# Kernel optimization log

Measured on AMD Instinct MI355X. Metric: run time of the kernel, lower is better.

## Reference

```python
import jax, jax.numpy as jnp
import numpy as np

# dims (match init_kwargs / input_specs)
B, T, IN, H, OUT, BR = 128, 250, 700, 512, 20, 4
VTH, DT, WARMUP = 1.0, 1.0, 10


@jax.custom_vjp
def spike_fn(v):
    # Heaviside spike with surrogate gradient (ActFun_adp style)
    return (v > 0.0).astype(v.dtype)

def _spike_fwd(v):
    return spike_fn(v), v

def _spike_bwd(v, g):
    gamma, lens = 0.5, 0.5  # gaussian surrogate
    return (g * gamma * jnp.exp(-v * v / (2.0 * lens * lens)),)

spike_fn.defvjp(_spike_fwd, _spike_bwd)


def make_mask(rng, out_dim, in_dim, branch):
    # each output neuron's branch j sees a disjoint random slice of inputs
    m = np.zeros((out_dim * branch, in_dim), np.float32)
    seg = in_dim // branch
    for i in range(out_dim):
        perm = rng.permutation(in_dim)
        for j in range(branch):
            m[i * branch + j, perm[j * seg:(j + 1) * seg]] = 1.0
    return jnp.asarray(m)


def setup_inputs() -> dict:
    key = jax.random.key(0)
    ks = jax.random.split(key, 12)
    rng = np.random.default_rng(0)
    lim1 = 1.0 / np.sqrt(IN)
    lim2 = 1.0 / np.sqrt(H)
    return {
        "x": jax.random.uniform(ks[0], (B, T, IN), dtype=jnp.float32),
        "W1": jax.random.uniform(ks[1], (H * BR, IN), minval=-lim1, maxval=lim1),
        "b1": jax.random.uniform(ks[2], (H * BR,), minval=-lim1, maxval=lim1),
        "tau_m1": jax.random.uniform(ks[3], (H,), minval=0.0, maxval=4.0),
        "tau_n1": jax.random.uniform(ks[4], (H, BR), minval=0.0, maxval=4.0),
        "mask1": make_mask(rng, H, IN, BR),
        "W2": jax.random.uniform(ks[5], (H * BR, H), minval=-lim2, maxval=lim2),
        "b2": jax.random.uniform(ks[6], (H * BR,), minval=-lim2, maxval=lim2),
        "tau_m2": jax.random.uniform(ks[7], (H,), minval=0.0, maxval=4.0),
        "tau_n2": jax.random.uniform(ks[8], (H, BR), minval=0.0, maxval=4.0),
        "mask2": make_mask(rng, H, H, BR),
        "Wo": jax.random.uniform(ks[9], (OUT, H), minval=-lim2, maxval=lim2),
        "bo": jax.random.uniform(ks[10], (OUT,), minval=-lim2, maxval=lim2),
        "tau_mo": jax.random.uniform(ks[11], (OUT,), minval=0.0, maxval=4.0),
    }


def reference(x, W1, b1, tau_m1, tau_n1, mask1, W2, b2, tau_m2, tau_n2, mask2, Wo, bo, tau_mo):
    beta1 = jax.nn.sigmoid(tau_n1)   # [H,BR] dendritic decay
    alpha1 = jax.nn.sigmoid(tau_m1)  # [H]   membrane decay
    beta2 = jax.nn.sigmoid(tau_n2)
    alpha2 = jax.nn.sigmoid(tau_m2)
    alpha_o = jax.nn.sigmoid(tau_mo)  # [OUT]
    Wm1 = W1 * mask1  # dendritic branch connectivity mask
    Wm2 = W2 * mask2
    Bsz = x.shape[0]
    Hd, Br = tau_n1.shape
    Od = tau_mo.shape[0]

    init = (jnp.zeros((Bsz, Hd, Br)), jnp.zeros((Bsz, Hd)), jnp.zeros((Bsz, Hd)),
            jnp.zeros((Bsz, Hd, Br)), jnp.zeros((Bsz, Hd)), jnp.zeros((Bsz, Hd)),
            jnp.zeros((Bsz, Od)))

    def step(c, xt):
        d1, m1, s1, d2, m2, s2, mo = c
        # layer 1: dendritic filter then LIF membrane with soft reset
        d1 = beta1 * d1 + (1.0 - beta1) * (xt @ Wm1.T + b1).reshape(Bsz, Hd, Br)
        m1 = m1 * alpha1 + (1.0 - alpha1) * DT * d1.sum(-1) - VTH * s1
        s1 = spike_fn(m1 - VTH)
        # layer 2
        d2 = beta2 * d2 + (1.0 - beta2) * (s1 @ Wm2.T + b2).reshape(Bsz, Hd, Br)
        m2 = m2 * alpha2 + (1.0 - alpha2) * DT * d2.sum(-1) - VTH * s2
        s2 = spike_fn(m2 - VTH)
        # leaky readout integrator (no spiking)
        mo = mo * alpha_o + (1.0 - alpha_o) * DT * (s2 @ Wo.T + bo)
        return (d1, m1, s1, d2, m2, s2, mo), jax.nn.softmax(mo, axis=1)

    _, ys = jax.lax.scan(step, init, jnp.swapaxes(x, 0, 1))  # ys: [T,B,OUT]
    # readout_mode == 'sum_softmax': skip steps i <= warmup_steps, sum the rest
    return ys[WARMUP + 1:].sum(0)
```

## Files before the change

### kernel.cpp

```cpp
#include <hip/hip_runtime.h>
#include <math.h>
#include <stdint.h>

#define B_    128
#define T_    250
#define IN_   700
#define INP_  704
#define H_    512
#define OUT_  20
#define BR_   4
#define HB_   2048
#define WARM_ 10
#define VTH_  1.0f
#define TC_   125
#define TP_   128
#define MP_   16384

typedef __attribute__((ext_vector_type(8)))  _Float16 half8;
typedef __attribute__((ext_vector_type(4)))  float f32x4;
typedef __attribute__((ext_vector_type(16))) float f32x16;
typedef __attribute__((ext_vector_type(4)))  int i32x4;
typedef __attribute__((ext_vector_type(16))) int i32x16;
typedef const __attribute__((address_space(1))) void* gptr_t;
typedef __attribute__((address_space(3))) void* lptr_t;

__global__ __launch_bounds__(256)
void w1prep_kernel(const float* __restrict__ W, const float* __restrict__ M,
                   _Float16* __restrict__ w0, _Float16* __restrict__ w1) {
    int i = blockIdx.x * 256 + threadIdx.x;
    if (i >= HB_ * INP_) return;
    int r = i / INP_, c = i - r * INP_;
    float v = (c < IN_) ? W[(size_t)r * IN_ + c] * M[(size_t)r * IN_ + c] : 0.f;
    _Float16 h0 = (_Float16)v;
    w0[i] = h0;
    w1[i] = (_Float16)(v - (float)h0);
}

__global__ __launch_bounds__(256)
void w2prep_kernel(const float* __restrict__ W, const float* __restrict__ M,
                   int8_t* __restrict__ p2, int8_t* __restrict__ p1,
                   int8_t* __restrict__ p0) {
    int i = blockIdx.x * 256 + threadIdx.x;
    if (i >= HB_ * H_) return;
    float v = W[i] * M[i];
    int q = (int)lrintf(v * 67108864.f);
    int b0 = (int)(int8_t)(q & 0xFF);  q = (q - b0) >> 8;
    int b1 = (int)(int8_t)(q & 0xFF);  int b2 = (q - b1) >> 8;
    p0[i] = (int8_t)b0; p1[i] = (int8_t)b1; p2[i] = (int8_t)b2;
}

__global__ __launch_bounds__(256)
void woprep_kernel(const float* __restrict__ Wo, _Float16* __restrict__ wo0,
                   _Float16* __restrict__ wo1) {
    int i = blockIdx.x * 256 + threadIdx.x;
    if (i >= 32 * H_) return;
    int n = i >> 9;
    float v = (n < OUT_) ? Wo[(size_t)n * H_ + (i & (H_ - 1))] : 0.f;
    _Float16 h0 = (_Float16)v;
    wo0[i] = h0;
    wo1[i] = (_Float16)(v - (float)h0);
}

__global__ __launch_bounds__(256)
void convx_kernel(const float* __restrict__ x, _Float16* __restrict__ x0,
                  _Float16* __restrict__ x1, int t0) {
    int i = blockIdx.x * 256 + threadIdx.x;
    if (i >= MP_ * INP_) return;
    int r = i / INP_, c = i - r * INP_;
    int bb = r >> 7, tl = r & (TP_ - 1);
    float v = (tl < TC_ && c < IN_) ? x[((size_t)bb * T_ + t0 + tl) * IN_ + c] : 0.f;
    _Float16 h0 = (_Float16)v;
    x0[i] = h0;
    x1[i] = (_Float16)(v - (float)h0);
}

__global__ void zero_kernel(float* __restrict__ p, int n4) {
    int i = blockIdx.x * blockDim.x + threadIdx.x;
    if (i < n4) ((float4*)p)[i] = make_float4(0.f, 0.f, 0.f, 0.f);
}

__global__ __launch_bounds__(256)
void l1_fused_kernel(const _Float16* __restrict__ x0, const _Float16* __restrict__ x1,
                     const _Float16* __restrict__ w0, const _Float16* __restrict__ w1,
                     const float* __restrict__ bias,
                     float* __restrict__ dst, float* __restrict__ mst,
                     float* __restrict__ spst, int8_t* __restrict__ sout,
                     const float* __restrict__ tau_m, const float* __restrict__ tau_n) {
    __shared__ alignas(16) char SMEM[69632];
    _Float16* S    = (_Float16*)SMEM;
    float*    curS = (float*)SMEM;
    int8_t*   sbuf = (int8_t*)(SMEM + 65536);

    const int tid  = threadIdx.x;
    const int wave = tid >> 6, lane = tid & 63;
    const int bb = blockIdx.y;
    const int bm = bb * TP_, bn = blockIdx.x * 128;

    const int    srow  = tid >> 2;
    const int    skoff = (((tid & 3) ^ ((srow >> 1) & 3)) * 8);
    const size_t aoff0 = (size_t)(bm + srow) * INP_ + skoff;
    const size_t aoff1 = aoff0 + (size_t)64 * INP_;
    const size_t boff0 = (size_t)(bn + srow) * INP_ + skoff;
    const size_t boff1 = boff0 + (size_t)64 * INP_;
    const int lo = wave * 512;

    const int wm = wave & 1, wn = wave >> 1;
    const int row = lane & 31;
    const int khq = lane >> 5;
    const int key = (lane >> 1) & 3;
    const int cK0 = ((0 + khq) ^ key) * 8;
    const int cK1 = ((2 + khq) ^ key) * 8;

    f32x16 acc[2][2] = {};

    auto stage = [&](int kt, int base) {
        const int k0 = kt * 32;
        _Float16* Sb = S + base;
        __builtin_amdgcn_global_load_lds((gptr_t)(x0 + aoff0 + k0), (lptr_t)(Sb + lo),          16, 0, 0);
        __builtin_amdgcn_global_load_lds((gptr_t)(x0 + aoff1 + k0), (lptr_t)(Sb + 2048  + lo),  16, 0, 0);
        __builtin_amdgcn_global_load_lds((gptr_t)(x1 + aoff0 + k0), (lptr_t)(Sb + 4096  + lo),  16, 0, 0);
        __builtin_amdgcn_global_load_lds((gptr_t)(x1 + aoff1 + k0), (lptr_t)(Sb + 6144  + lo),  16, 0, 0);
        __builtin_amdgcn_global_load_lds((gptr_t)(w0 + boff0 + k0), (lptr_t)(Sb + 8192  + lo),  16, 0, 0);
        __builtin_amdgcn_global_load_lds((gptr_t)(w0 + boff1 + k0), (lptr_t)(Sb + 10240 + lo),  16, 0, 0);
        __builtin_amdgcn_global_load_lds((gptr_t)(w1 + boff0 + k0), (lptr_t)(Sb + 12288 + lo),  16, 0, 0);
        __builtin_amdgcn_global_load_lds((gptr_t)(w1 + boff1 + k0), (lptr_t)(Sb + 14336 + lo),  16, 0, 0);
    };

    auto compute = [&](int base) {
        const _Float16* A0b = S + base;
        const _Float16* A1b = A0b + 4096;
        const _Float16* B0b = A0b + 8192;
        const _Float16* B1b = A0b + 12288;
        half8 a0f[2][2], a1f[2][2], b0f[2][2], b1f[2][2];
#pragma unroll
        for (int mt = 0; mt < 2; mt++) {
            const _Float16* ar = &A0b[(wm * 64 + mt * 32 + row) * 32];
            a0f[mt][0] = *(const half8*)&ar[cK0];
            a0f[mt][1] = *(const half8*)&ar[cK1];
        }
#pragma unroll
        for (int nt = 0; nt < 2; nt++) {
            const _Float16* br = &B0b[(wn * 64 + nt * 32 + row) * 32];
            b0f[nt][0] = *(const half8*)&br[cK0];
            b0f[nt][1] = *(const half8*)&br[cK1];
        }
        __builtin_amdgcn_s_setprio(1);
#pragma unroll
        for (int ks = 0; ks < 2; ks++)
#pragma unroll
            for (int mt = 0; mt < 2; mt++)
#pragma unroll
                for (int nt = 0; nt < 2; nt++)
                    acc[mt][nt] = __builtin_amdgcn_mfma_f32_32x32x16_f16(
                        a0f[mt][ks], b0f[nt][ks], acc[mt][nt], 0, 0, 0);
        __builtin_amdgcn_s_setprio(0);
#pragma unroll
        for (int nt = 0; nt < 2; nt++) {
            const _Float16* br = &B1b[(wn * 64 + nt * 32 + row) * 32];
            b1f[nt][0] = *(const half8*)&br[cK0];
            b1f[nt][1] = *(const half8*)&br[cK1];
        }
        __builtin_amdgcn_s_setprio(1);
#pragma unroll
        for (int ks = 0; ks < 2; ks++)
#pragma unroll
            for (int mt = 0; mt < 2; mt++)
#pragma unroll
                for (int nt = 0; nt < 2; nt++)
                    acc[mt][nt] = __builtin_amdgcn_mfma_f32_32x32x16_f16(
                        a0f[mt][ks], b1f[nt][ks], acc[mt][nt], 0, 0, 0);
        __builtin_amdgcn_s_setprio(0);
#pragma unroll
        for (int mt = 0; mt < 2; mt++) {
            const _Float16* ar = &A1b[(wm * 64 + mt * 32 + row) * 32];
            a1f[mt][0] = *(const half8*)&ar[cK0];
            a1f[mt][1] = *(const half8*)&ar[cK1];
        }
        __builtin_amdgcn_s_setprio(1);
#pragma unroll
        for (int ks = 0; ks < 2; ks++)
#pragma unroll
            for (int mt = 0; mt < 2; mt++)
#pragma unroll
                for (int nt = 0; nt < 2; nt++)
                    acc[mt][nt] = __builtin_amdgcn_mfma_f32_32x32x16_f16(
                        a1f[mt][ks], b0f[nt][ks], acc[mt][nt], 0, 0, 0);
        __builtin_amdgcn_s_setprio(0);
    };

    stage(0, 0);
    asm volatile("s_waitcnt vmcnt(0)" ::: "memory");
    __builtin_amdgcn_s_barrier();

    int cur = 0;
    for (int kt = 0; kt < INP_ / 32 - 1; kt++) {
        const int base = cur * 16384;
        stage(kt + 1, base ^ 16384);
        compute(base);
        asm volatile("s_waitcnt vmcnt(0) lgkmcnt(0)" ::: "memory");
        __builtin_amdgcn_s_barrier();
        cur ^= 1;
    }
    compute(cur * 16384);
    __syncthreads();

    const int col = lane & 31;
    const int rb  = 4 * (lane >> 5);
#pragma unroll
    for (int nt = 0; nt < 2; nt++) {
        const int lcol = wn * 64 + nt * 32 + col;
        const float bv = bias[bn + lcol];
#pragma unroll
        for (int mt = 0; mt < 2; mt++) {
#pragma unroll
            for (int reg = 0; reg < 16; reg++) {
                const int trow = wm * 64 + mt * 32 + (reg & 3) + 8 * (reg >> 2) + rb;
                curS[trow * 128 + lcol] = acc[mt][nt][reg] + bv;
            }
        }
    }
    __syncthreads();

    if (tid < 32) {
        const int hg   = blockIdx.x * 32 + tid;
        const int sidx = bb * H_ + hg;
        float alpha = 1.f / (1.f + expf(-tau_m[hg]));
        float4 tn = ((const float4*)tau_n)[hg];
        float4 beta;
        beta.x = 1.f / (1.f + expf(-tn.x));
        beta.y = 1.f / (1.f + expf(-tn.y));
        beta.z = 1.f / (1.f + expf(-tn.z));
        beta.w = 1.f / (1.f + expf(-tn.w));
        float4 d = ((const float4*)dst)[sidx];
        float m = mst[sidx];
        float sp = spst[sidx];
#pragma unroll 5
        for (int t = 0; t < TC_; t++) {
            float4 c = ((const float4*)(curS + t * 128))[tid];
            d.x = beta.x * d.x + (1.f - beta.x) * c.x;
            d.y = beta.y * d.y + (1.f - beta.y) * c.y;
            d.z = beta.z * d.z + (1.f - beta.z) * c.z;
            d.w = beta.w * d.w + (1.f - beta.w) * c.w;
            float s4 = ((d.x + d.y) + d.z) + d.w;
            m = m * alpha + (1.f - alpha) * s4 - VTH_ * sp;
            sp = (m > VTH_) ? 1.f : 0.f;
            sbuf[t * 32 + tid] = (int8_t)(m > VTH_);
        }
        sbuf[125 * 32 + tid] = 0; sbuf[126 * 32 + tid] = 0; sbuf[127 * 32 + tid] = 0;
        ((float4*)dst)[sidx] = d;
        mst[sidx] = m;
        spst[sidx] = sp;
    }
    __syncthreads();
    if (tid < TP_) {
        int4* dp = (int4*)&sout[((size_t)(bm + tid)) * H_ + blockIdx.x * 32];
        const int4* sp4 = (const int4*)&sbuf[tid * 32];
        dp[0] = sp4[0]; dp[1] = sp4[1];
    }
}

__global__ __launch_bounds__(256)
void l2_fused_kernel(const int8_t* __restrict__ A,
                     const int8_t* __restrict__ p2, const int8_t* __restrict__ p1,
                     const int8_t* __restrict__ p0,
                     const float* __restrict__ bias,
                     float* __restrict__ dst, float* __restrict__ mst,
                     float* __restrict__ spst, _Float16* __restrict__ sout,
                     const float* __restrict__ tau_m, const float* __restrict__ tau_n) {
    __shared__ alignas(16) char SMEM[73728];
    int8_t*   S    = (int8_t*)SMEM;
    float*    curS = (float*)SMEM;
    _Float16* sbuf = (_Float16*)(SMEM + 65536);

    const int tid  = threadIdx.x;
    const int wave = tid >> 6, lane = tid & 63;
    const int bb = blockIdx.y;
    const int bm = bb * TP_, bn = blockIdx.x * 128;

    const int    srow  = tid >> 2;
    const int    skoff = (((tid & 3) ^ ((srow >> 1) & 3)) * 16);
    const size_t aoff0 = (size_t)(bm + srow) * H_ + skoff;
    const size_t aoff1 = aoff0 + (size_t)64 * H_;
    const size_t boff0 = (size_t)(bn + srow) * H_ + skoff;
    const size_t boff1 = boff0 + (size_t)64 * H_;
    const int lo = wave * 1024;

    const int wm = wave & 1, wn = wave >> 1;
    const int row = lane & 31;
    const int khq = lane >> 5;
    const int key = (lane >> 1) & 3;
    const int cK0 = ((0 + khq) ^ key) * 16;
    const int cK1 = ((2 + khq) ^ key) * 16;

    i32x16 acc[2][2] = {};

    auto stage = [&](int i, int base) {
        const int s  = i >> 3;
        const int k0 = (i & 7) * 64;
        const int8_t* pw = (s == 0) ? p2 : (s == 1) ? p1 : p0;
        int8_t* Sb = S + base;
        __builtin_amdgcn_global_load_lds((gptr_t)(A  + aoff0 + k0), (lptr_t)(Sb + lo),          16, 0, 0);
        __builtin_amdgcn_global_load_lds((gptr_t)(A  + aoff1 + k0), (lptr_t)(Sb + 4096  + lo),  16, 0, 0);
        __builtin_amdgcn_global_load_lds((gptr_t)(pw + boff0 + k0), (lptr_t)(Sb + 8192  + lo),  16, 0, 0);
        __builtin_amdgcn_global_load_lds((gptr_t)(pw + boff1 + k0), (lptr_t)(Sb + 12288 + lo),  16, 0, 0);
    };

    auto compute = [&](int base) {
        const int8_t* Ab = S + base;
        const int8_t* Bb = Ab + 8192;
        i32x4 af[2][2], bf[2][2];
#pragma unroll
        for (int mt = 0; mt < 2; mt++) {
            const int8_t* ar = &Ab[(wm * 64 + mt * 32 + row) * 64];
            af[mt][0] = *(const i32x4*)&ar[cK0];
            af[mt][1] = *(const i32x4*)&ar[cK1];
        }
#pragma unroll
        for (int nt = 0; nt < 2; nt++) {
            const int8_t* br = &Bb[(wn * 64 + nt * 32 + row) * 64];
            bf[nt][0] = *(const i32x4*)&br[cK0];
            bf[nt][1] = *(const i32x4*)&br[cK1];
        }
        __builtin_amdgcn_s_setprio(1);
#pragma unroll
        for (int ks = 0; ks < 2; ks++)
#pragma unroll
            for (int mt = 0; mt < 2; mt++)
#pragma unroll
                for (int nt = 0; nt < 2; nt++)
                    acc[mt][nt] = __builtin_amdgcn_mfma_i32_32x32x32_i8(
                        af[mt][ks], bf[nt][ks], acc[mt][nt], 0, 0, 0);
        __builtin_amdgcn_s_setprio(0);
    };

    stage(0, 0);
    asm volatile("s_waitcnt vmcnt(0)" ::: "memory");
    __builtin_amdgcn_s_barrier();

    int cur = 0;
    for (int i = 0; i < 23; i++) {
        const int base = cur * 16384;
        stage(i + 1, base ^ 16384);
        if (i == 8 || i == 16) {
#pragma unroll
            for (int mt = 0; mt < 2; mt++)
#pragma unroll
                for (int nt = 0; nt < 2; nt++) acc[mt][nt] *= 256;
        }
        compute(base);
        asm volatile("s_waitcnt vmcnt(0) lgkmcnt(0)" ::: "memory");
        __builtin_amdgcn_s_barrier();
        cur ^= 1;
    }
    compute(cur * 16384);
    __syncthreads();

    const float scale = 1.f / 67108864.f;
    const int col = lane & 31;
    const int rb  = 4 * (lane >> 5);
#pragma unroll
    for (int nt = 0; nt < 2; nt++) {
        const int lcol = wn * 64 + nt * 32 + col;
        const float bv = bias[bn + lcol];
#pragma unroll
        for (int mt = 0; mt < 2; mt++) {
#pragma unroll
            for (int reg = 0; reg < 16; reg++) {
                const int trow = wm * 64 + mt * 32 + (reg & 3) + 8 * (reg >> 2) + rb;
                curS[trow * 128 + lcol] = (float)acc[mt][nt][reg] * scale + bv;
            }
        }
    }
    __syncthreads();

    if (tid < 32) {
        const int hg   = blockIdx.x * 32 + tid;
        const int sidx = bb * H_ + hg;
        float alpha = 1.f / (1.f + expf(-tau_m[hg]));
        float4 tn = ((const float4*)tau_n)[hg];
        float4 beta;
        beta.x = 1.f / (1.f + expf(-tn.x));
        beta.y = 1.f / (1.f + expf(-tn.y));
        beta.z = 1.f / (1.f + expf(-tn.z));
        beta.w = 1.f / (1.f + expf(-tn.w));
        float4 d = ((const float4*)dst)[sidx];
        float m = mst[sidx];
        float sp = spst[sidx];
#pragma unroll 5
        for (int t = 0; t < TC_; t++) {
            float4 c = ((const float4*)(curS + t * 128))[tid];
            d.x = beta.x * d.x + (1.f - beta.x) * c.x;
            d.y = beta.y * d.y + (1.f - beta.y) * c.y;
            d.z = beta.z * d.z + (1.f - beta.z) * c.z;
            d.w = beta.w * d.w + (1.f - beta.w) * c.w;
            float s4 = ((d.x + d.y) + d.z) + d.w;
            m = m * alpha + (1.f - alpha) * s4 - VTH_ * sp;
            sp = (m > VTH_) ? 1.f : 0.f;
            sbuf[t * 32 + tid] = (_Float16)sp;
        }
        sbuf[125 * 32 + tid] = (_Float16)0.f;
        sbuf[126 * 32 + tid] = (_Float16)0.f;
        sbuf[127 * 32 + tid] = (_Float16)0.f;
        ((float4*)dst)[sidx] = d;
        mst[sidx] = m;
        spst[sidx] = sp;
    }
    __syncthreads();
    if (tid < TP_) {
        int4* dp = (int4*)&sout[((size_t)(bm + tid)) * H_ + blockIdx.x * 32];
        const int4* sp4 = (const int4*)&sbuf[tid * 32];
        dp[0] = sp4[0]; dp[1] = sp4[1]; dp[2] = sp4[2]; dp[3] = sp4[3];
    }
}

__global__ __launch_bounds__(256)
void rdot_mfma_kernel(const _Float16* __restrict__ s2c, const _Float16* __restrict__ wo0,
                      const _Float16* __restrict__ wo1, const float* __restrict__ bo,
                      float* __restrict__ curo, int t0) {
    __shared__ alignas(16) _Float16 S[2 * 6144];
    const int tid  = threadIdx.x;
    const int wave = tid >> 6, lane = tid & 63;
    const int bm = blockIdx.x * 128;

    const int    srow  = tid >> 2;
    const int    skoff = (((tid & 3) ^ ((srow >> 1) & 3)) * 8);
    const size_t aoff0 = (size_t)(bm + srow) * H_ + skoff;
    const size_t aoff1 = aoff0 + (size_t)64 * H_;
    const _Float16* bsrc = (wave < 2) ? wo0 : wo1;
    const int bw = wave & 1;
    const size_t boff = (size_t)(bw * 16 + (lane >> 2)) * H_
                      + ((lane & 3) ^ ((lane >> 3) & 3)) * 8;
    const int loA = wave * 512;
    const int loB = 4096 + (wave >> 1) * 1024 + bw * 512;

    const int fr = lane & 15;
    const int key = (lane >> 1) & 3;
    const int cK  = (((lane >> 4) ^ key) * 8);

    f32x4 acc[2][2] = {};

    auto stage = [&](int kt, int base) {
        const int k0 = kt * 32;
        _Float16* Sb = S + base;
        __builtin_amdgcn_global_load_lds((gptr_t)(s2c + aoff0 + k0),  (lptr_t)(Sb + loA),        16, 0, 0);
        __builtin_amdgcn_global_load_lds((gptr_t)(s2c + aoff1 + k0),  (lptr_t)(Sb + 2048 + loA), 16, 0, 0);
        __builtin_amdgcn_global_load_lds((gptr_t)(bsrc + boff + k0),  (lptr_t)(Sb + loB),        16, 0, 0);
    };

    auto compute = [&](int base) {
        const _Float16* Ab  = S + base;
        const _Float16* B0b = Ab + 4096;
        const _Float16* B1b = Ab + 5120;
        half8 af[2], b0[2], b1[2];
#pragma unroll
        for (int mi = 0; mi < 2; mi++)
            af[mi] = *(const half8*)&Ab[(wave * 32 + mi * 16 + fr) * 32 + cK];
#pragma unroll
        for (int ni = 0; ni < 2; ni++) {
            b0[ni] = *(const half8*)&B0b[(ni * 16 + fr) * 32 + cK];
            b1[ni] = *(const half8*)&B1b[(ni * 16 + fr) * 32 + cK];
        }
        __builtin_amdgcn_s_setprio(1);
#pragma unroll
        for (int mi = 0; mi < 2; mi++)
#pragma unroll
            for (int ni = 0; ni < 2; ni++) {
                acc[mi][ni] = __builtin_amdgcn_mfma_f32_16x16x32_f16(af[mi], b0[ni], acc[mi][ni], 0, 0, 0);
                acc[mi][ni] = __builtin_amdgcn_mfma_f32_16x16x32_f16(af[mi], b1[ni], acc[mi][ni], 0, 0, 0);
            }
        __builtin_amdgcn_s_setprio(0);
    };

    stage(0, 0);
    asm volatile("s_waitcnt vmcnt(0)" ::: "memory");
    __builtin_amdgcn_s_barrier();

    int cur = 0;
    for (int kt = 0; kt < H_ / 32 - 1; kt++) {
        const int base = cur * 6144;
        stage(kt + 1, base ^ 6144);
        compute(base);
        asm volatile("s_waitcnt vmcnt(0) lgkmcnt(0)" ::: "memory");
        __builtin_amdgcn_s_barrier();
        cur ^= 1;
    }
    compute(cur * 6144);

    const int cc = lane & 15;
    const int cr = (lane >> 4) * 4;
#pragma unroll
    for (int ni = 0; ni < 2; ni++) {
        const int gc = ni * 16 + cc;
        if (gc < OUT_) {
            const float bv = bo[gc];
#pragma unroll
            for (int mi = 0; mi < 2; mi++) {
#pragma unroll
                for (int r = 0; r < 4; r++) {
                    const int gr = bm + wave * 32 + mi * 16 + cr + r;
                    const int bb = gr >> 7, tl = gr & (TP_ - 1);
                    if (tl < TC_)
                        curo[((size_t)bb * T_ + t0 + tl) * OUT_ + gc] = acc[mi][ni][r] + bv;
                }
            }
        }
    }
}

#define RT_SEG 12
#define RT_LEN 21

__global__ __launch_bounds__(256)
void readout_kernel(const float* __restrict__ curo, const float* __restrict__ tau_mo,
                    float* __restrict__ out) {
    __shared__ float moS[T_ * OUT_];
    __shared__ float segA[RT_SEG][OUT_];
    __shared__ float segU[RT_SEG][OUT_];
    __shared__ float pre[RT_SEG][OUT_];
    __shared__ float accS[OUT_];
    const int b = blockIdx.x;
    const int tid = threadIdx.x;
    const float* cb = curo + (size_t)b * T_ * OUT_;

    const int o = tid % OUT_;
    const int sg = tid / OUT_;
    const float ao = 1.f / (1.f + expf(-tau_mo[o]));

    if (tid < RT_SEG * OUT_) {
        int t0 = sg * RT_LEN;
        int t1 = min(T_, t0 + RT_LEN);
        float u = 0.f, Ap = 1.f;
        for (int t = t0; t < t1; t++) {
            u = ao * u + (1.f - ao) * cb[t * OUT_ + o];
            Ap *= ao;
        }
        segU[sg][o] = u; segA[sg][o] = Ap;
    }
    if (tid < OUT_) accS[tid] = 0.f;
    __syncthreads();
    if (tid < OUT_) {
        float m = 0.f;
        for (int s = 0; s < RT_SEG; s++) {
            pre[s][tid] = m;
            m = segA[s][tid] * m + segU[s][tid];
        }
    }
    __syncthreads();
    if (tid < RT_SEG * OUT_) {
        int t0 = sg * RT_LEN;
        int t1 = min(T_, t0 + RT_LEN);
        float m = pre[sg][o];
        for (int t = t0; t < t1; t++) {
            m = ao * m + (1.f - ao) * cb[t * OUT_ + o];
            moS[t * OUT_ + o] = m;
        }
    }
    __syncthreads();
    if (tid >= WARM_ + 1 && tid < T_) {
        int t = tid;
        float mx = -3.0e38f;
#pragma unroll
        for (int o2 = 0; o2 < OUT_; o2++) mx = fmaxf(mx, moS[t * OUT_ + o2]);
        float es[OUT_]; float se = 0.f;
#pragma unroll
        for (int o2 = 0; o2 < OUT_; o2++) {
            float e = expf(moS[t * OUT_ + o2] - mx);
            es[o2] = e; se += e;
        }
        float inv = 1.f / se;
#pragma unroll
        for (int o2 = 0; o2 < OUT_; o2++) atomicAdd(&accS[o2], es[o2] * inv);
    }
    __syncthreads();
    if (tid < OUT_) out[(size_t)b * OUT_ + tid] = accS[tid];
}

extern "C" void kernel_launch(void* const* d_in, const int* in_sizes, int n_in,
                              void* d_out, int out_size, void* d_ws, size_t ws_size,
                              hipStream_t stream) {
    const float* x      = (const float*)d_in[0];
    const float* W1     = (const float*)d_in[1];
    const float* b1     = (const float*)d_in[2];
    const float* tau_m1 = (const float*)d_in[3];
    const float* tau_n1 = (const float*)d_in[4];
    const float* mask1  = (const float*)d_in[5];
    const float* W2     = (const float*)d_in[6];
    const float* b2     = (const float*)d_in[7];
    const float* tau_m2 = (const float*)d_in[8];
    const float* tau_n2 = (const float*)d_in[9];
    const float* mask2  = (const float*)d_in[10];
    const float* Wo     = (const float*)d_in[11];
    const float* bo     = (const float*)d_in[12];
    const float* tau_mo = (const float*)d_in[13];
    float* out = (float*)d_out;

    char* p = (char*)d_ws;
    auto alloc = [&](size_t bytes) { char* r = p; p += (bytes + 255) & ~(size_t)255; return r; };
    _Float16* w10 = (_Float16*)alloc((size_t)HB_ * INP_ * 2);
    _Float16* w11 = (_Float16*)alloc((size_t)HB_ * INP_ * 2);
    int8_t*   q2  = (int8_t*)alloc((size_t)HB_ * H_);
    int8_t*   q1  = (int8_t*)alloc((size_t)HB_ * H_);
    int8_t*   q0  = (int8_t*)alloc((size_t)HB_ * H_);
    _Float16* wo0 = (_Float16*)alloc((size_t)32 * H_ * 2);
    _Float16* wo1 = (_Float16*)alloc((size_t)32 * H_ * 2);
    _Float16* xc0 = (_Float16*)alloc((size_t)MP_ * INP_ * 2);
    _Float16* xc1 = (_Float16*)alloc((size_t)MP_ * INP_ * 2);
    int8_t*   s1c = (int8_t*)alloc((size_t)MP_ * H_);
    _Float16* s2c = (_Float16*)alloc((size_t)MP_ * H_ * 2);
    float* curo   = (float*)alloc((size_t)B_ * T_ * OUT_ * 4);
    float* st     = (float*)alloc((size_t)786432 * 4);
    float* d1  = st;
    float* m1  = d1 + (size_t)B_ * H_ * BR_;
    float* sp1 = m1 + (size_t)B_ * H_;
    float* d2  = sp1 + (size_t)B_ * H_;
    float* m2  = d2 + (size_t)B_ * H_ * BR_;
    float* sp2 = m2 + (size_t)B_ * H_;

    w1prep_kernel<<<(HB_ * INP_ + 255) / 256, 256, 0, stream>>>(W1, mask1, w10, w11);
    w2prep_kernel<<<(HB_ * H_ + 255) / 256, 256, 0, stream>>>(W2, mask2, q2, q1, q0);
    woprep_kernel<<<(32 * H_ + 255) / 256, 256, 0, stream>>>(Wo, wo0, wo1);
    zero_kernel<<<(786432 / 4 + 255) / 256, 256, 0, stream>>>(st, 786432 / 4);

    dim3 gg(HB_ / 128, B_);
    for (int c = 0; c < 2; c++) {
        const int t0 = c * TC_;
        convx_kernel<<<(MP_ * INP_) / 256, 256, 0, stream>>>(x, xc0, xc1, t0);
        l1_fused_kernel<<<gg, 256, 0, stream>>>(xc0, xc1, w10, w11, b1,
                                                d1, m1, sp1, s1c, tau_m1, tau_n1);
        l2_fused_kernel<<<gg, 256, 0, stream>>>(s1c, q2, q1, q0, b2,
                                                d2, m2, sp2, s2c, tau_m2, tau_n2);
        rdot_mfma_kernel<<<MP_ / 128, 256, 0, stream>>>(s2c, wo0, wo1, bo, curo, t0);
    }
    readout_kernel<<<B_, 256, 0, stream>>>(curo, tau_mo, out);
}
```

Before: 785.3 us.

## Widen fused layer GEMM tiles to 256 columns and register-stage the A operand

Both fused layer kernels now compute a 128x256 output tile per block instead of 128x128, which halves the grid and doubles reuse of the activation tile across weight columns. In layer 1 the activation tile is loaded once into registers and written to a single LDS buffer, while only the weights are double-buffered through direct global-to-LDS loads. The scan epilogue is split into two halves that run one after another, each over 32 neurons. This trades a larger register footprint (8 accumulator tiles), more LDS per block and fewer blocks for less redundant A-operand traffic. The serial epilogue now runs twice per block on a single wave, which adds latency.

```diff
diff --git a/kernel.cpp b/kernel.cpp
--- a/kernel.cpp
+++ b/kernel.cpp
@@ -24,6 +24,8 @@
 typedef const __attribute__((address_space(1))) void* gptr_t;
 typedef __attribute__((address_space(3))) void* lptr_t;
 
+#define SB0() __builtin_amdgcn_sched_barrier(0)
+
 __global__ __launch_bounds__(256)
 void w1prep_kernel(const float* __restrict__ W, const float* __restrict__ M,
                    _Float16* __restrict__ w0, _Float16* __restrict__ w1) {
@@ -86,23 +88,20 @@
                      float* __restrict__ dst, float* __restrict__ mst,
                      float* __restrict__ spst, int8_t* __restrict__ sout,
                      const float* __restrict__ tau_m, const float* __restrict__ tau_n) {
-    __shared__ alignas(16) char SMEM[69632];
-    _Float16* S    = (_Float16*)SMEM;
-    float*    curS = (float*)SMEM;
-    int8_t*   sbuf = (int8_t*)(SMEM + 65536);
+    __shared__ alignas(16) char SMEM[81920];
+    float*  curS = (float*)(SMEM + 16384);
+    int8_t* sbuf = (int8_t*)SMEM;
 
     const int tid  = threadIdx.x;
     const int wave = tid >> 6, lane = tid & 63;
     const int bb = blockIdx.y;
-    const int bm = bb * TP_, bn = blockIdx.x * 128;
-
-    const int    srow  = tid >> 2;
-    const int    skoff = (((tid & 3) ^ ((srow >> 1) & 3)) * 8);
-    const size_t aoff0 = (size_t)(bm + srow) * INP_ + skoff;
-    const size_t aoff1 = aoff0 + (size_t)64 * INP_;
-    const size_t boff0 = (size_t)(bn + srow) * INP_ + skoff;
-    const size_t boff1 = boff0 + (size_t)64 * INP_;
-    const int lo = wave * 512;
+    const int bm = bb * TP_, bn = blockIdx.x * 256;
+
+    const int srow   = tid >> 2;
+    const int chunk  = tid & 3;
+    const int wchunk = chunk ^ ((srow >> 1) & 3);
+    const size_t boff = (size_t)(bn + srow) * INP_ + wchunk * 8;
+    const size_t aoff = (size_t)(bm + srow) * INP_ + chunk * 8;
 
     const int wm = wave & 1, wn = wave >> 1;
     const int row = lane & 31;
@@ -111,151 +110,168 @@
     const int cK0 = ((0 + khq) ^ key) * 8;
     const int cK1 = ((2 + khq) ^ key) * 8;
 
-    f32x16 acc[2][2] = {};
-
-    auto stage = [&](int kt, int base) {
+    f32x16 acc[2][4] = {};
+    int4 aR[4];
+
+    auto stageB = [&](int kt, int base) {
         const int k0 = kt * 32;
-        _Float16* Sb = S + base;
-        __builtin_amdgcn_global_load_lds((gptr_t)(x0 + aoff0 + k0), (lptr_t)(Sb + lo),          16, 0, 0);
-        __builtin_amdgcn_global_load_lds((gptr_t)(x0 + aoff1 + k0), (lptr_t)(Sb + 2048  + lo),  16, 0, 0);
-        __builtin_amdgcn_global_load_lds((gptr_t)(x1 + aoff0 + k0), (lptr_t)(Sb + 4096  + lo),  16, 0, 0);
-        __builtin_amdgcn_global_load_lds((gptr_t)(x1 + aoff1 + k0), (lptr_t)(Sb + 6144  + lo),  16, 0, 0);
-        __builtin_amdgcn_global_load_lds((gptr_t)(w0 + boff0 + k0), (lptr_t)(Sb + 8192  + lo),  16, 0, 0);
-        __builtin_amdgcn_global_load_lds((gptr_t)(w0 + boff1 + k0), (lptr_t)(Sb + 10240 + lo),  16, 0, 0);
-        __builtin_amdgcn_global_load_lds((gptr_t)(w1 + boff0 + k0), (lptr_t)(Sb + 12288 + lo),  16, 0, 0);
-        __builtin_amdgcn_global_load_lds((gptr_t)(w1 + boff1 + k0), (lptr_t)(Sb + 14336 + lo),  16, 0, 0);
+        char* Sb = SMEM + 16384 + base;
+#pragma unroll
+        for (int g = 0; g < 4; g++) {
+            __builtin_amdgcn_global_load_lds((gptr_t)(w0 + boff + (size_t)g * 64 * INP_ + k0),
+                                             (lptr_t)(Sb + g * 4096 + wave * 1024), 16, 0, 0);
+            __builtin_amdgcn_global_load_lds((gptr_t)(w1 + boff + (size_t)g * 64 * INP_ + k0),
+                                             (lptr_t)(Sb + 16384 + g * 4096 + wave * 1024), 16, 0, 0);
+        }
+    };
+
+    auto loadA = [&](int kt) {
+        const int k0 = kt * 32;
+        aR[0] = *(const int4*)(x0 + aoff + k0);
+        aR[1] = *(const int4*)(x0 + aoff + (size_t)64 * INP_ + k0);
+        aR[2] = *(const int4*)(x1 + aoff + k0);
+        aR[3] = *(const int4*)(x1 + aoff + (size_t)64 * INP_ + k0);
+    };
+
+    auto writeA = [&]() {
+        char* d = SMEM + srow * 64 + wchunk * 16;
+        *(int4*)(d)         = aR[0];
+        *(int4*)(d + 4096)  = aR[1];
+        *(int4*)(d + 8192)  = aR[2];
+        *(int4*)(d + 12288) = aR[3];
     };
 
     auto compute = [&](int base) {
-        const _Float16* A0b = S + base;
-        const _Float16* A1b = A0b + 4096;
-        const _Float16* B0b = A0b + 8192;
-        const _Float16* B1b = A0b + 12288;
-        half8 a0f[2][2], a1f[2][2], b0f[2][2], b1f[2][2];
+        const _Float16* A0s = (const _Float16*)SMEM;
+        const _Float16* A1s = (const _Float16*)(SMEM + 8192);
+        const _Float16* W0b = (const _Float16*)(SMEM + 16384 + base);
+        const _Float16* W1b = W0b + 8192;
+        half8 a0f[2][2], a1f[2][2];
 #pragma unroll
         for (int mt = 0; mt < 2; mt++) {
-            const _Float16* ar = &A0b[(wm * 64 + mt * 32 + row) * 32];
-            a0f[mt][0] = *(const half8*)&ar[cK0];
-            a0f[mt][1] = *(const half8*)&ar[cK1];
-        }
-#pragma unroll
-        for (int nt = 0; nt < 2; nt++) {
-            const _Float16* br = &B0b[(wn * 64 + nt * 32 + row) * 32];
-            b0f[nt][0] = *(const half8*)&br[cK0];
-            b0f[nt][1] = *(const half8*)&br[cK1];
-        }
-        __builtin_amdgcn_s_setprio(1);
-#pragma unroll
-        for (int ks = 0; ks < 2; ks++)
-#pragma unroll
-            for (int mt = 0; mt < 2; mt++)
-#pragma unroll
-                for (int nt = 0; nt < 2; nt++)
+            const _Float16* r0 = &A0s[(wm * 64 + mt * 32 + row) * 32];
+            const _Float16* r1 = &A1s[(wm * 64 + mt * 32 + row) * 32];
+            a0f[mt][0] = *(const half8*)&r0[cK0];
+            a0f[mt][1] = *(const half8*)&r0[cK1];
+            a1f[mt][0] = *(const half8*)&r1[cK0];
+            a1f[mt][1] = *(const half8*)&r1[cK1];
+        }
+#pragma unroll
+        for (int nt = 0; nt < 4; nt++) {
+            const _Float16* b0r = &W0b[(wn * 128 + nt * 32 + row) * 32];
+            const _Float16* b1r = &W1b[(wn * 128 + nt * 32 + row) * 32];
+            half8 b0[2], b1[2];
+            b0[0] = *(const half8*)&b0r[cK0];
+            b0[1] = *(const half8*)&b0r[cK1];
+            b1[0] = *(const half8*)&b1r[cK0];
+            b1[1] = *(const half8*)&b1r[cK1];
+            __builtin_amdgcn_s_setprio(1);
+#pragma unroll
+            for (int ks = 0; ks < 2; ks++)
+#pragma unroll
+                for (int mt = 0; mt < 2; mt++)
                     acc[mt][nt] = __builtin_amdgcn_mfma_f32_32x32x16_f16(
-                        a0f[mt][ks], b0f[nt][ks], acc[mt][nt], 0, 0, 0);
-        __builtin_amdgcn_s_setprio(0);
-#pragma unroll
-        for (int nt = 0; nt < 2; nt++) {
-            const _Float16* br = &B1b[(wn * 64 + nt * 32 + row) * 32];
-            b1f[nt][0] = *(const half8*)&br[cK0];
-            b1f[nt][1] = *(const half8*)&br[cK1];
-        }
-        __builtin_amdgcn_s_setprio(1);
-#pragma unroll
-        for (int ks = 0; ks < 2; ks++)
-#pragma unroll
-            for (int mt = 0; mt < 2; mt++)
-#pragma unroll
-                for (int nt = 0; nt < 2; nt++)
+                        a0f[mt][ks], b0[ks], acc[mt][nt], 0, 0, 0);
+#pragma unroll
+            for (int ks = 0; ks < 2; ks++)
+#pragma unroll
+                for (int mt = 0; mt < 2; mt++)
                     acc[mt][nt] = __builtin_amdgcn_mfma_f32_32x32x16_f16(
-                        a0f[mt][ks], b1f[nt][ks], acc[mt][nt], 0, 0, 0);
-        __builtin_amdgcn_s_setprio(0);
-#pragma unroll
-        for (int mt = 0; mt < 2; mt++) {
-            const _Float16* ar = &A1b[(wm * 64 + mt * 32 + row) * 32];
-            a1f[mt][0] = *(const half8*)&ar[cK0];
-            a1f[mt][1] = *(const half8*)&ar[cK1];
-        }
-        __builtin_amdgcn_s_setprio(1);
-#pragma unroll
-        for (int ks = 0; ks < 2; ks++)
-#pragma unroll
-            for (int mt = 0; mt < 2; mt++)
-#pragma unroll
-                for (int nt = 0; nt < 2; nt++)
+                        a0f[mt][ks], b1[ks], acc[mt][nt], 0, 0, 0);
+#pragma unroll
+            for (int ks = 0; ks < 2; ks++)
+#pragma unroll
+                for (int mt = 0; mt < 2; mt++)
                     acc[mt][nt] = __builtin_amdgcn_mfma_f32_32x32x16_f16(
-                        a1f[mt][ks], b0f[nt][ks], acc[mt][nt], 0, 0, 0);
-        __builtin_amdgcn_s_setprio(0);
-    };
-
-    stage(0, 0);
+                        a1f[mt][ks], b0[ks], acc[mt][nt], 0, 0, 0);
+            __builtin_amdgcn_s_setprio(0);
+        }
+    };
+
+    stageB(0, 0);
+    loadA(0);
+    SB0();
     asm volatile("s_waitcnt vmcnt(0)" ::: "memory");
+    writeA();
+    asm volatile("s_waitcnt lgkmcnt(0)" ::: "memory");
     __builtin_amdgcn_s_barrier();
 
     int cur = 0;
+#pragma unroll 1
     for (int kt = 0; kt < INP_ / 32 - 1; kt++) {
-        const int base = cur * 16384;
-        stage(kt + 1, base ^ 16384);
+        const int base = cur * 32768;
+        stageB(kt + 1, base ^ 32768);
+        loadA(kt + 1);
+        SB0();
         compute(base);
-        asm volatile("s_waitcnt vmcnt(0) lgkmcnt(0)" ::: "memory");
+        __builtin_amdgcn_s_barrier();
+        asm volatile("s_waitcnt vmcnt(0)" ::: "memory");
+        writeA();
+        asm volatile("s_waitcnt lgkmcnt(0)" ::: "memory");
         __builtin_amdgcn_s_barrier();
         cur ^= 1;
     }
-    compute(cur * 16384);
+    compute(cur * 32768);
     __syncthreads();
 
     const int col = lane & 31;
     const int rb  = 4 * (lane >> 5);
-#pragma unroll
-    for (int nt = 0; nt < 2; nt++) {
-        const int lcol = wn * 64 + nt * 32 + col;
-        const float bv = bias[bn + lcol];
-#pragma unroll
-        for (int mt = 0; mt < 2; mt++) {
-#pragma unroll
-            for (int reg = 0; reg < 16; reg++) {
-                const int trow = wm * 64 + mt * 32 + (reg & 3) + 8 * (reg >> 2) + rb;
-                curS[trow * 128 + lcol] = acc[mt][nt][reg] + bv;
+#pragma unroll 1
+    for (int half = 0; half < 2; half++) {
+        if (wn == half) {
+#pragma unroll
+            for (int nt = 0; nt < 4; nt++) {
+                const int lcol = nt * 32 + col;
+                const float bv = bias[bn + half * 128 + lcol];
+#pragma unroll
+                for (int mt = 0; mt < 2; mt++) {
+#pragma unroll
+                    for (int reg = 0; reg < 16; reg++) {
+                        const int trow = wm * 64 + mt * 32 + (reg & 3) + 8 * (reg >> 2) + rb;
+                        curS[trow * 128 + lcol] = acc[mt][nt][reg] + bv;
+                    }
+                }
             }
         }
-    }
-    __syncthreads();
-
-    if (tid < 32) {
-        const int hg   = blockIdx.x * 32 + tid;
-        const int sidx = bb * H_ + hg;
-        float alpha = 1.f / (1.f + expf(-tau_m[hg]));
-        float4 tn = ((const float4*)tau_n)[hg];
-        float4 beta;
-        beta.x = 1.f / (1.f + expf(-tn.x));
-        beta.y = 1.f / (1.f + expf(-tn.y));
-        beta.z = 1.f / (1.f + expf(-tn.z));
-        beta.w = 1.f / (1.f + expf(-tn.w));
-        float4 d = ((const float4*)dst)[sidx];
-        float m = mst[sidx];
-        float sp = spst[sidx];
+        __syncthreads();
+        if (tid < 32) {
+            const int hg   = blockIdx.x * 64 + half * 32 + tid;
+            const int sidx = bb * H_ + hg;
+            float alpha = 1.f / (1.f + expf(-tau_m[hg]));
+            float4 tn = ((const float4*)tau_n)[hg];
+            float4 beta;
+            beta.x = 1.f / (1.f + expf(-tn.x));
+            beta.y = 1.f / (1.f + expf(-tn.y));
+            beta.z = 1.f / (1.f + expf(-tn.z));
+            beta.w = 1.f / (1.f + expf(-tn.w));
+            float4 d = ((const float4*)dst)[sidx];
+            float m = mst[sidx];
+            float sp = spst[sidx];
 #pragma unroll 5
-        for (int t = 0; t < TC_; t++) {
-            float4 c = ((const float4*)(curS + t * 128))[tid];
-            d.x = beta.x * d.x + (1.f - beta.x) * c.x;
-            d.y = beta.y * d.y + (1.f - beta.y) * c.y;
-            d.z = beta.z * d.z + (1.f - beta.z) * c.z;
-            d.w = beta.w * d.w + (1.f - beta.w) * c.w;
-            float s4 = ((d.x + d.y) + d.z) + d.w;
-            m = m * alpha + (1.f - alpha) * s4 - VTH_ * sp;
-            sp = (m > VTH_) ? 1.f : 0.f;
-            sbuf[t * 32 + tid] = (int8_t)(m > VTH_);
-        }
-        sbuf[125 * 32 + tid] = 0; sbuf[126 * 32 + tid] = 0; sbuf[127 * 32 + tid] = 0;
-        ((float4*)dst)[sidx] = d;
-        mst[sidx] = m;
-        spst[sidx] = sp;
-    }
-    __syncthreads();
+            for (int t = 0; t < TC_; t++) {
+                float4 c = ((const float4*)(curS + t * 128))[tid];
+                d.x = beta.x * d.x + (1.f - beta.x) * c.x;
+                d.y = beta.y * d.y + (1.f - beta.y) * c.y;
+                d.z = beta.z * d.z + (1.f - beta.z) * c.z;
+                d.w = beta.w * d.w + (1.f - beta.w) * c.w;
+                float s4 = ((d.x + d.y) + d.z) + d.w;
+                m = m * alpha + (1.f - alpha) * s4 - VTH_ * sp;
+                sp = (m > VTH_) ? 1.f : 0.f;
+                sbuf[t * 64 + half * 32 + tid] = (int8_t)(m > VTH_);
+            }
+            sbuf[125 * 64 + half * 32 + tid] = 0;
+            sbuf[126 * 64 + half * 32 + tid] = 0;
+            sbuf[127 * 64 + half * 32 + tid] = 0;
+            ((float4*)dst)[sidx] = d;
+            mst[sidx] = m;
+            spst[sidx] = sp;
+        }
+        __syncthreads();
+    }
     if (tid < TP_) {
-        int4* dp = (int4*)&sout[((size_t)(bm + tid)) * H_ + blockIdx.x * 32];
-        const int4* sp4 = (const int4*)&sbuf[tid * 32];
-        dp[0] = sp4[0]; dp[1] = sp4[1];
+        int4* dp = (int4*)&sout[((size_t)(bm + tid)) * H_ + blockIdx.x * 64];
+        const int4* s4 = (const int4*)&sbuf[tid * 64];
+        dp[0] = s4[0]; dp[1] = s4[1]; dp[2] = s4[2]; dp[3] = s4[3];
     }
 }
 
@@ -267,23 +283,20 @@
                      float* __restrict__ dst, float* __restrict__ mst,
                      float* __restrict__ spst, _Float16* __restrict__ sout,
                      const float* __restrict__ tau_m, const float* __restrict__ tau_n) {
-    __shared__ alignas(16) char SMEM[73728];
-    int8_t*   S    = (int8_t*)SMEM;
+    __shared__ alignas(16) char SMEM[81920];
     float*    curS = (float*)SMEM;
     _Float16* sbuf = (_Float16*)(SMEM + 65536);
 
     const int tid  = threadIdx.x;
     const int wave = tid >> 6, lane = tid & 63;
     const int bb = blockIdx.y;
-    const int bm = bb * TP_, bn = blockIdx.x * 128;
-
-    const int    srow  = tid >> 2;
-    const int    skoff = (((tid & 3) ^ ((srow >> 1) & 3)) * 16);
-    const size_t aoff0 = (size_t)(bm + srow) * H_ + skoff;
-    const size_t aoff1 = aoff0 + (size_t)64 * H_;
-    const size_t boff0 = (size_t)(bn + srow) * H_ + skoff;
-    const size_t boff1 = boff0 + (size_t)64 * H_;
-    const int lo = wave * 1024;
+    const int bm = bb * TP_, bn = blockIdx.x * 256;
+
+    const int srow   = tid >> 2;
+    const int chunk  = tid & 3;
+    const int wchunk = chunk ^ ((srow >> 1) & 3);
+    const size_t aoff = (size_t)(bm + srow) * H_ + wchunk * 16;
+    const size_t boff = (size_t)(bn + srow) * H_ + wchunk * 16;
 
     const int wm = wave & 1, wn = wave >> 1;
     const int row = lane & 31;
@@ -292,23 +305,27 @@
     const int cK0 = ((0 + khq) ^ key) * 16;
     const int cK1 = ((2 + khq) ^ key) * 16;
 
-    i32x16 acc[2][2] = {};
+    i32x16 acc[2][4] = {};
 
     auto stage = [&](int i, int base) {
         const int s  = i >> 3;
         const int k0 = (i & 7) * 64;
         const int8_t* pw = (s == 0) ? p2 : (s == 1) ? p1 : p0;
-        int8_t* Sb = S + base;
-        __builtin_amdgcn_global_load_lds((gptr_t)(A  + aoff0 + k0), (lptr_t)(Sb + lo),          16, 0, 0);
-        __builtin_amdgcn_global_load_lds((gptr_t)(A  + aoff1 + k0), (lptr_t)(Sb + 4096  + lo),  16, 0, 0);
-        __builtin_amdgcn_global_load_lds((gptr_t)(pw + boff0 + k0), (lptr_t)(Sb + 8192  + lo),  16, 0, 0);
-        __builtin_amdgcn_global_load_lds((gptr_t)(pw + boff1 + k0), (lptr_t)(Sb + 12288 + lo),  16, 0, 0);
+        char* Sb = SMEM + base;
+#pragma unroll
+        for (int g = 0; g < 2; g++)
+            __builtin_amdgcn_global_load_lds((gptr_t)(A + aoff + (size_t)g * 64 * H_ + k0),
+                                             (lptr_t)(Sb + g * 4096 + wave * 1024), 16, 0, 0);
+#pragma unroll
+        for (int g = 0; g < 4; g++)
+            __builtin_amdgcn_global_load_lds((gptr_t)(pw + boff + (size_t)g * 64 * H_ + k0),
+                                             (lptr_t)(Sb + 8192 + g * 4096 + wave * 1024), 16, 0, 0);
     };
 
     auto compute = [&](int base) {
-        const int8_t* Ab = S + base;
+        const int8_t* Ab = (const int8_t*)(SMEM + base);
         const int8_t* Bb = Ab + 8192;
-        i32x4 af[2][2], bf[2][2];
+        i32x4 af[2][2];
 #pragma unroll
         for (int mt = 0; mt < 2; mt++) {
             const int8_t* ar = &Ab[(wm * 64 + mt * 32 + row) * 64];
@@ -316,21 +333,20 @@
             af[mt][1] = *(const i32x4*)&ar[cK1];
         }
 #pragma unroll
-        for (int nt = 0; nt < 2; nt++) {
-            const int8_t* br = &Bb[(wn * 64 + nt * 32 + row) * 64];
-            bf[nt][0] = *(const i32x4*)&br[cK0];
-            bf[nt][1] = *(const i32x4*)&br[cK1];
-        }
-        __builtin_amdgcn_s_setprio(1);
-#pragma unroll
-        for (int ks = 0; ks < 2; ks++)
-#pragma unroll
-            for (int mt = 0; mt < 2; mt++)
-#pragma unroll
-                for (int nt = 0; nt < 2; nt++)
+        for (int nt = 0; nt < 4; nt++) {
+            const int8_t* br = &Bb[(wn * 128 + nt * 32 + row) * 64];
+            i32x4 bf[2];
+            bf[0] = *(const i32x4*)&br[cK0];
+            bf[1] = *(const i32x4*)&br[cK1];
+            __builtin_amdgcn_s_setprio(1);
+#pragma unroll
+            for (int ks = 0; ks < 2; ks++)
+#pragma unroll
+                for (int mt = 0; mt < 2; mt++)
                     acc[mt][nt] = __builtin_amdgcn_mfma_i32_32x32x32_i8(
-                        af[mt][ks], bf[nt][ks], acc[mt][nt], 0, 0, 0);
-        __builtin_amdgcn_s_setprio(0);
+                        af[mt][ks], bf[ks], acc[mt][nt], 0, 0, 0);
+            __builtin_amdgcn_s_setprio(0);
+        }
     };
 
     stage(0, 0);
@@ -338,78 +354,84 @@
     __builtin_amdgcn_s_barrier();
 
     int cur = 0;
+#pragma unroll 1
     for (int i = 0; i < 23; i++) {
-        const int base = cur * 16384;
-        stage(i + 1, base ^ 16384);
+        const int base = cur * 24576;
+        stage(i + 1, base ^ 24576);
         if (i == 8 || i == 16) {
 #pragma unroll
             for (int mt = 0; mt < 2; mt++)
 #pragma unroll
-                for (int nt = 0; nt < 2; nt++) acc[mt][nt] *= 256;
+                for (int nt = 0; nt < 4; nt++) acc[mt][nt] *= 256;
         }
         compute(base);
         asm volatile("s_waitcnt vmcnt(0) lgkmcnt(0)" ::: "memory");
         __builtin_amdgcn_s_barrier();
         cur ^= 1;
     }
-    compute(cur * 16384);
+    compute(cur * 24576);
     __syncthreads();
 
     const float scale = 1.f / 67108864.f;
     const int col = lane & 31;
     const int rb  = 4 * (lane >> 5);
-#pragma unroll
-    for (int nt = 0; nt < 2; nt++) {
-        const int lcol = wn * 64 + nt * 32 + col;
-        const float bv = bias[bn + lcol];
-#pragma unroll
-        for (int mt = 0; mt < 2; mt++) {
-#pragma unroll
-            for (int reg = 0; reg < 16; reg++) {
-                const int trow = wm * 64 + mt * 32 + (reg & 3) + 8 * (reg >> 2) + rb;
-                curS[trow * 128 + lcol] = (float)acc[mt][nt][reg] * scale + bv;
+#pragma unroll 1
+    for (int half = 0; half < 2; half++) {
+        if (wn == half) {
+#pragma unroll
+            for (int nt = 0; nt < 4; nt++) {
+                const int lcol = nt * 32 + col;
+                const float bv = bias[bn + half * 128 + lcol];
+#pragma unroll
+                for (int mt = 0; mt < 2; mt++) {
+#pragma unroll
+                    for (int reg = 0; reg < 16; reg++) {
+                        const int trow = wm * 64 + mt * 32 + (reg & 3) + 8 * (reg >> 2) + rb;
+                        curS[trow * 128 + lcol] = (float)acc[mt][nt][reg] * scale + bv;
+                    }
+                }
             }
         }
-    }
-    __syncthreads();
-
-    if (tid < 32) {
-        const int hg   = blockIdx.x * 32 + tid;
-        const int sidx = bb * H_ + hg;
-        float alpha = 1.f / (1.f + expf(-tau_m[hg]));
-        float4 tn = ((const float4*)tau_n)[hg];
-        float4 beta;
-        beta.x = 1.f / (1.f + expf(-tn.x));
-        beta.y = 1.f / (1.f + expf(-tn.y));
-        beta.z = 1.f / (1.f + expf(-tn.z));
-        beta.w = 1.f / (1.f + expf(-tn.w));
-        float4 d = ((const float4*)dst)[sidx];
-        float m = mst[sidx];
-        float sp = spst[sidx];
+        __syncthreads();
+        if (tid < 32) {
+            const int hg   = blockIdx.x * 64 + half * 32 + tid;
+            const int sidx = bb * H_ + hg;
+            float alpha = 1.f / (1.f + expf(-tau_m[hg]));
+            float4 tn = ((const float4*)tau_n)[hg];
+            float4 beta;
+            beta.x = 1.f / (1.f + expf(-tn.x));
+            beta.y = 1.f / (1.f + expf(-tn.y));
+            beta.z = 1.f / (1.f + expf(-tn.z));
+            beta.w = 1.f / (1.f + expf(-tn.w));
+            float4 d = ((const float4*)dst)[sidx];
+            float m = mst[sidx];
+            float sp = spst[sidx];
 #pragma unroll 5
-        for (int t = 0; t < TC_; t++) {
-            float4 c = ((const float4*)(curS + t * 128))[tid];
-            d.x = beta.x * d.x + (1.f - beta.x) * c.x;
-            d.y = beta.y * d.y + (1.f - beta.y) * c.y;
-            d.z = beta.z * d.z + (1.f - beta.z) * c.z;
-            d.w = beta.w * d.w + (1.f - beta.w) * c.w;
-            float s4 = ((d.x + d.y) + d.z) + d.w;
-            m = m * alpha + (1.f - alpha) * s4 - VTH_ * sp;
-            sp = (m > VTH_) ? 1.f : 0.f;
-            sbuf[t * 32 + tid] = (_Float16)sp;
-        }
-        sbuf[125 * 32 + tid] = (_Float16)0.f;
-        sbuf[126 * 32 + tid] = (_Float16)0.f;
-        sbuf[127 * 32 + tid] = (_Float16)0.f;
-        ((float4*)dst)[sidx] = d;
-        mst[sidx] = m;
-        spst[sidx] = sp;
-    }
-    __syncthreads();
+            for (int t = 0; t < TC_; t++) {
+                float4 c = ((const float4*)(curS + t * 128))[tid];
+                d.x = beta.x * d.x + (1.f - beta.x) * c.x;
+                d.y = beta.y * d.y + (1.f - beta.y) * c.y;
+                d.z = beta.z * d.z + (1.f - beta.z) * c.z;
+                d.w = beta.w * d.w + (1.f - beta.w) * c.w;
+                float s4 = ((d.x + d.y) + d.z) + d.w;
+                m = m * alpha + (1.f - alpha) * s4 - VTH_ * sp;
+                sp = (m > VTH_) ? 1.f : 0.f;
+                sbuf[t * 64 + half * 32 + tid] = (_Float16)sp;
+            }
+            sbuf[125 * 64 + half * 32 + tid] = (_Float16)0.f;
+            sbuf[126 * 64 + half * 32 + tid] = (_Float16)0.f;
+            sbuf[127 * 64 + half * 32 + tid] = (_Float16)0.f;
+            ((float4*)dst)[sidx] = d;
+            mst[sidx] = m;
+            spst[sidx] = sp;
+        }
+        __syncthreads();
+    }
     if (tid < TP_) {
-        int4* dp = (int4*)&sout[((size_t)(bm + tid)) * H_ + blockIdx.x * 32];
-        const int4* sp4 = (const int4*)&sbuf[tid * 32];
-        dp[0] = sp4[0]; dp[1] = sp4[1]; dp[2] = sp4[2]; dp[3] = sp4[3];
+        int4* dp = (int4*)&sout[((size_t)(bm + tid)) * H_ + blockIdx.x * 64];
+        const int4* s4 = (const int4*)&sbuf[tid * 64];
+#pragma unroll
+        for (int j = 0; j < 8; j++) dp[j] = s4[j];
     }
 }
 
@@ -621,7 +643,7 @@
     woprep_kernel<<<(32 * H_ + 255) / 256, 256, 0, stream>>>(Wo, wo0, wo1);
     zero_kernel<<<(786432 / 4 + 255) / 256, 256, 0, stream>>>(st, 786432 / 4);
 
-    dim3 gg(HB_ / 128, B_);
+    dim3 gg(HB_ / 256, B_);
     for (int c = 0; c < 2; c++) {
         const int t0 = c * TC_;
         convx_kernel<<<(MP_ * INP_) / 256, 256, 0, stream>>>(x, xc0, xc1, t0);
```

Result: slower. 1.226 ms (+56.2%).
